# Performance work log

Hardware: AMD Instinct MI355X
Metric: run time of the kernel (lower is better)

Reference implementation:

```python
import jax, jax.numpy as jnp
import numpy as np

N_NODES = 10000
N_EDGES = 80000
N_GRAPHS = 64
H, D = 4, 512          # num_heads, out_feats
EMB = 768
HFEAT = 512
NCLS = 2
SLOPE = 0.2            # DGL GATConv default negative_slope
BN_EPS = 1e-5


def setup_inputs() -> dict:
    key = jax.random.key(0)
    ks = jax.random.split(key, 24)
    f32 = jnp.float32
    rn = lambda k, s, sc=0.02: jax.random.normal(k, s, dtype=f32) * sc
    inp = {
        "node_feat": jax.random.normal(ks[0], (N_NODES, EMB), dtype=f32),
        "func_feat": jax.random.normal(ks[1], (N_NODES, EMB), dtype=f32),
        "W1": rn(ks[2], (EMB, H * D)),
        "al1": rn(ks[3], (H, D), 0.1),
        "ar1": rn(ks[4], (H, D), 0.1),
        "b1": jnp.zeros((H * D,), f32),
        "W2": rn(ks[5], (H * D, H * D)),
        "al2": rn(ks[6], (H, D), 0.1),
        "ar2": rn(ks[7], (H, D), 0.1),
        "b2": jnp.zeros((H * D,), f32),
        "Wfc": rn(ks[8], (H * D, HFEAT)),
        "bfc": jnp.zeros((HFEAT,), f32),
        "Wfco": rn(ks[9], (EMB, HFEAT)),
        "bfco": jnp.zeros((HFEAT,), f32),
        "Wh": rn(ks[10], (8, HFEAT, HFEAT)),
        "bh": jnp.zeros((8, HFEAT), f32),
        "gamma": jnp.ones((HFEAT,), f32),
        "beta": jnp.zeros((HFEAT,), f32),
        "Whfc": rn(ks[11], (HFEAT, HFEAT)),
        "bhfc": jnp.zeros((HFEAT,), f32),
        "Wf": rn(ks[12], (HFEAT, NCLS)),
        "bf": jnp.zeros((NCLS,), f32),
        "src": jax.random.randint(ks[13], (N_EDGES,), 0, N_NODES),
        "dst": jax.random.randint(ks[14], (N_EDGES,), 0, N_NODES),
        "graph_id": jnp.sort(jax.random.randint(ks[15], (N_NODES,), 0, N_GRAPHS)),
    }
    return inp


def gat_conv(h, W, al, ar, b, src, dst):
    """DGL GATConv (eval mode): fc -> per-head attention logits -> edge
    softmax over incoming edges -> scatter-sum -> +bias. Returns (N, H*D)."""
    feat = (h @ W).reshape(-1, H, D)                      # (N,H,D)
    el = jnp.einsum('nhd,hd->nh', feat, al)               # (N,H)
    er = jnp.einsum('nhd,hd->nh', feat, ar)
    e = jax.nn.leaky_relu(el[src] + er[dst], SLOPE)       # (E,H)
    emax = jax.ops.segment_max(e, dst, num_segments=N_NODES)
    ex = jnp.exp(e - emax[dst])
    den = jax.ops.segment_sum(ex, dst, num_segments=N_NODES)
    a = ex / den[dst]                                     # edge softmax (E,H)
    msg = feat[src] * a[:, :, None]                       # (E,H,D) gather+weight
    out = jax.ops.segment_sum(msg, dst, num_segments=N_NODES)
    return (out + b.reshape(1, H, D)).reshape(-1, H * D)


def reference(node_feat, func_feat, W1, al1, ar1, b1, W2, al2, ar2, b2,
              Wfc, bfc, Wfco, bfco, Wh, bh, gamma, beta, Whfc, bhfc,
              Wf, bf, src, dst, graph_id):
    h = gat_conv(node_feat, W1, al1, ar1, b1, src, dst)   # (N, 2048)
    h = gat_conv(h, W2, al2, ar2, b2, src, dst)           # (N, 2048)
    h = jax.nn.elu(h @ Wfc + bfc)                         # (N, 512)
    h_func = jax.nn.elu(func_feat @ Wfco + bfco)          # (N, 512)
    for i in range(8):
        h = jax.nn.elu(h @ Wh[i] + bh[i])
        h_func = jax.nn.elu(h_func @ Wh[i] + bh[i])       # dead for output (as in torch)
    counts = jax.ops.segment_sum(jnp.ones((N_NODES,), h.dtype), graph_id,
                                 num_segments=N_GRAPHS)
    hg = jax.ops.segment_sum(h, graph_id, num_segments=N_GRAPHS)
    hg = hg / jnp.maximum(counts, 1.0)[:, None]           # dgl.mean_nodes (G, 512)
    # BatchNorm1d eval with running_mean=0, running_var=1
    hg = hg / jnp.sqrt(1.0 + BN_EPS) * gamma + beta
    hg = jax.nn.elu(hg @ Whfc + bhfc)
    return hg @ Wf + bf                                   # (G, NCLS)
```

## Files before the change

### kernel.cpp

```cpp
#include <hip/hip_runtime.h>
#include <hip/hip_bf16.h>
#include <math.h>

#define N_NODES 10000
#define N_EDGES 80000
#define N_GRAPHS 64
#define NH 4
#define HD 512
#define HDTOT 2048
#define EMB 768
#define HFEAT 512

typedef _Float16 half8 __attribute__((ext_vector_type(8)));
typedef _Float16 half4 __attribute__((ext_vector_type(4)));
typedef float f32x4 __attribute__((ext_vector_type(4)));

__device__ __forceinline__ void gload_lds16(const void* g, void* l) {
  __builtin_amdgcn_global_load_lds(
      (const __attribute__((address_space(1))) unsigned int*)g,
      (__attribute__((address_space(3))) unsigned int*)l, 16, 0, 0);
}


template <int BM>
__global__ __launch_bounds__(256) void gemm_f16_kernel(
    const _Float16* __restrict__ A, const _Float16* __restrict__ BTs,
    const float* __restrict__ bias, _Float16* __restrict__ C,
    int M, int N, int K, int act) {
  constexpr int WR = (BM == 128) ? 2 : 1;
  constexpr int WC = 4 / WR;
  constexpr int MI = (BM / WR) / 16;
  constexpr int NI = (128 / WC) / 16;

  __shared__ _Float16 As[BM * 32];
  __shared__ _Float16 Bs[128 * 32];

  const int bn = blockIdx.x * 128, bm = blockIdx.y * BM;
  const int t = threadIdx.x;
  const int lane = t & 63, wave = t >> 6;
  const int wr = wave / WC, wc = wave % WC;
  const int m0 = wr * (BM / WR), n0 = wc * (128 / WC);
  const int fr = lane & 15, fq = lane >> 4;

  f32x4 acc[MI][NI];
#pragma unroll
  for (int i = 0; i < MI; ++i)
#pragma unroll
    for (int j = 0; j < NI; ++j) acc[i][j] = (f32x4){0.f, 0.f, 0.f, 0.f};

  for (int k0 = 0; k0 < K; k0 += 32) {
    __syncthreads();
#pragma unroll
    for (int it = 0; it < BM / 64; ++it) {
      int gid = it * 256 + t;
      int r = gid >> 2, q = gid & 3;
      int grow = bm + r;
      if (grow >= M) grow = M - 1;
      half8 v = *(const half8*)(A + (size_t)grow * K + k0 + q * 8);
      *(half8*)&As[r * 32 + (q ^ ((r >> 1) & 3)) * 8] = v;
    }
#pragma unroll
    for (int it = 0; it < 2; ++it) {
      int gid = it * 256 + t;
      int r = gid >> 2, q = gid & 3;
      gload_lds16(BTs + (size_t)(bn + r) * K + k0 + q * 8,
                  &Bs[(it * 256 + wave * 64) * 8]);
    }
    __syncthreads();

    half8 af[MI], bf[NI];
#pragma unroll
    for (int mi = 0; mi < MI; ++mi) {
      int m = m0 + mi * 16 + fr;
      af[mi] = *(const half8*)&As[m * 32 + (fq ^ ((m >> 1) & 3)) * 8];
    }
#pragma unroll
    for (int ni = 0; ni < NI; ++ni) {
      int n = n0 + ni * 16 + fr;
      bf[ni] = *(const half8*)&Bs[n * 32 + (fq ^ ((n >> 1) & 3)) * 8];
    }
#pragma unroll
    for (int mi = 0; mi < MI; ++mi)
#pragma unroll
      for (int ni = 0; ni < NI; ++ni)
        acc[mi][ni] = __builtin_amdgcn_mfma_f32_16x16x32_f16(
            af[mi], bf[ni], acc[mi][ni], 0, 0, 0);
  }
#pragma unroll
  for (int mi = 0; mi < MI; ++mi) {
#pragma unroll
    for (int ni = 0; ni < NI; ++ni) {
      int gcol = bn + n0 + ni * 16 + fr;
      float bb = bias ? bias[gcol] : 0.f;
#pragma unroll
      for (int j = 0; j < 4; ++j) {
        int grow = bm + m0 + mi * 16 + fq * 4 + j;
        if (grow < M) {
          float v = acc[mi][ni][j] + bb;
          if (act == 1) v = v > 0.f ? v : expm1f(v);
          C[(size_t)grow * N + gcol] = (_Float16)v;
        }
      }
    }
  }
}

__global__ __launch_bounds__(256) void hidden_fused_kernel(
    const _Float16* __restrict__ X, const _Float16* __restrict__ Wt,
    const float* __restrict__ bh, _Float16* __restrict__ Y, int M) {
  constexpr int AS = 516;
  __shared__ _Float16 act[32 * AS];
  __shared__ _Float16 Bs[512 * 32];
  const int bm = blockIdx.x * 32;
  const int t = threadIdx.x;
  const int lane = t & 63, wave = t >> 6;
  const int n0w = wave * 128;
  const int fr = lane & 15, fq = lane >> 4;

#pragma unroll
  for (int it = 0; it < 8; ++it) {
    int gid = it * 256 + t;
    int r = gid >> 6, g = gid & 63;
    int grow = bm + r;
    if (grow >= M) grow = M - 1;
    half8 v = *(const half8*)(X + (size_t)grow * HFEAT + g * 8);
    *(half8*)&act[r * AS + g * 8] = v;
  }

  for (int layer = 0; layer < 8; ++layer) {
    const _Float16* W = Wt + (size_t)layer * HFEAT * HFEAT;
    f32x4 acc[2][8];
#pragma unroll
    for (int i = 0; i < 2; ++i)
#pragma unroll
      for (int j = 0; j < 8; ++j) acc[i][j] = (f32x4){0.f, 0.f, 0.f, 0.f};

    for (int k0 = 0; k0 < HFEAT; k0 += 32) {
      __syncthreads();
#pragma unroll
      for (int it = 0; it < 8; ++it) {
        int gid = it * 256 + t;
        int r = gid >> 2, q = gid & 3;
        gload_lds16(W + (size_t)r * HFEAT + k0 + q * 8,
                    &Bs[(it * 256 + wave * 64) * 8]);
      }
      __syncthreads();
      half8 af[2], bf[8];
#pragma unroll
      for (int mi = 0; mi < 2; ++mi)
        af[mi] = *(const half8*)&act[(mi * 16 + fr) * AS + k0 + fq * 8];
#pragma unroll
      for (int ni = 0; ni < 8; ++ni) {
        int n = n0w + ni * 16 + fr;
        bf[ni] = *(const half8*)&Bs[n * 32 + (fq ^ ((n >> 1) & 3)) * 8];
      }
#pragma unroll
      for (int mi = 0; mi < 2; ++mi)
#pragma unroll
        for (int ni = 0; ni < 8; ++ni)
          acc[mi][ni] = __builtin_amdgcn_mfma_f32_16x16x32_f16(
              af[mi], bf[ni], acc[mi][ni], 0, 0, 0);
    }
    __syncthreads();
#pragma unroll
    for (int ni = 0; ni < 8; ++ni) {
      int n = n0w + ni * 16 + fr;
      float bb = bh[layer * HFEAT + n];
#pragma unroll
      for (int mi = 0; mi < 2; ++mi) {
#pragma unroll
        for (int j = 0; j < 4; ++j) {
          int m = mi * 16 + fq * 4 + j;
          float v = acc[mi][ni][j] + bb;
          v = v > 0.f ? v : expm1f(v);
          act[m * AS + n] = (_Float16)v;
        }
      }
    }
  }
  __syncthreads();
#pragma unroll
  for (int it = 0; it < 8; ++it) {
    int gid = it * 256 + t;
    int r = gid >> 6, g = gid & 63;
    if (bm + r < M)
      *(half8*)&Y[(size_t)(bm + r) * HFEAT + g * 8] =
          *(const half8*)&act[r * AS + g * 8];
  }
}

__global__ __launch_bounds__(256) void convert_wt_kernel(
    const float* __restrict__ W, _Float16* __restrict__ WT, int K, int N) {
  __shared__ float tile[32][33];
  W += (size_t)blockIdx.z * K * N;
  WT += (size_t)blockIdx.z * K * N;
  int k0 = blockIdx.x * 32, n0 = blockIdx.y * 32;
  int t = threadIdx.x;
  int r = t >> 3, c4 = (t & 7) * 4;
  float4 v = *(const float4*)(W + (size_t)(k0 + r) * N + n0 + c4);
  tile[r][c4 + 0] = v.x;
  tile[r][c4 + 1] = v.y;
  tile[r][c4 + 2] = v.z;
  tile[r][c4 + 3] = v.w;
  __syncthreads();
  float x0 = tile[c4 + 0][r], x1 = tile[c4 + 1][r];
  float x2 = tile[c4 + 2][r], x3 = tile[c4 + 3][r];
  int n = n0 + r;
  int q = c4 >> 3;
  int s = q ^ ((n >> 1) & 3);
  size_t o = (size_t)n * K + k0 + s * 8 + (c4 & 7);
  *(half4*)&WT[o] = (half4){(_Float16)x0, (_Float16)x1, (_Float16)x2, (_Float16)x3};
}

__global__ void convert_f32_f16_kernel(const float* __restrict__ x,
                                       _Float16* __restrict__ y, int n4) {
  int gid = blockIdx.x * blockDim.x + threadIdx.x;
  if (gid >= n4) return;
  float4 v = *(const float4*)(x + gid * 4);
  *(half4*)(y + gid * 4) =
      (half4){(_Float16)v.x, (_Float16)v.y, (_Float16)v.z, (_Float16)v.w};
}

__global__ void hist_kernel(const int* __restrict__ dst, int* __restrict__ cnt, int E) {
  int gid = blockIdx.x * blockDim.x + threadIdx.x;
  if (gid < E) atomicAdd(&cnt[dst[gid]], 1);
}

__global__ void scan_kernel(const int* __restrict__ cnt, int* __restrict__ row_ptr,
                            int* __restrict__ cursor, int n) {
  __shared__ int part[256];
  int t = threadIdx.x;
  int chunk = (n + 255) / 256;
  int s0 = t * chunk;
  int s1 = min(s0 + chunk, n);
  int sum = 0;
  for (int i = s0; i < s1; ++i) sum += cnt[i];
  part[t] = sum;
  __syncthreads();
  if (t == 0) {
    int acc = 0;
    for (int i = 0; i < 256; ++i) { int v = part[i]; part[i] = acc; acc += v; }
    row_ptr[n] = acc;
  }
  __syncthreads();
  int run = part[t];
  for (int i = s0; i < s1; ++i) {
    row_ptr[i] = run;
    cursor[i] = run;
    run += cnt[i];
  }
}

__global__ void scatter_kernel(const int* __restrict__ dst, int* __restrict__ cursor,
                               int* __restrict__ edge_idx, int E) {
  int gid = blockIdx.x * blockDim.x + threadIdx.x;
  if (gid < E) {
    int pos = atomicAdd(&cursor[dst[gid]], 1);
    edge_idx[pos] = gid;
  }
}

__global__ __launch_bounds__(256) void el_er_kernel(
    const _Float16* __restrict__ feat, const float* __restrict__ al,
    const float* __restrict__ ar, float* __restrict__ el, float* __restrict__ er) {
  int n = blockIdx.x;
  int t = threadIdx.x;
  int h = t >> 6, lane = t & 63;
  half8 f = *(const half8*)(feat + (size_t)n * HDTOT + h * HD + lane * 8);
  const float* ap = al + h * HD + lane * 8;
  const float* rp = ar + h * HD + lane * 8;
  float4 a0 = *(const float4*)ap, a1 = *(const float4*)(ap + 4);
  float4 r0 = *(const float4*)rp, r1 = *(const float4*)(rp + 4);
  float f0 = (float)f[0], f1 = (float)f[1], f2 = (float)f[2], f3 = (float)f[3];
  float f4 = (float)f[4], f5 = (float)f[5], f6 = (float)f[6], f7 = (float)f[7];
  float sl = f0 * a0.x + f1 * a0.y + f2 * a0.z + f3 * a0.w +
             f4 * a1.x + f5 * a1.y + f6 * a1.z + f7 * a1.w;
  float sr = f0 * r0.x + f1 * r0.y + f2 * r0.z + f3 * r0.w +
             f4 * r1.x + f5 * r1.y + f6 * r1.z + f7 * r1.w;
  for (int off = 32; off; off >>= 1) {
    sl += __shfl_down(sl, off);
    sr += __shfl_down(sr, off);
  }
  if (lane == 0) {
    el[n * NH + h] = sl;
    er[n * NH + h] = sr;
  }
}

__global__ void edge_e_kernel(const float* __restrict__ el, const float* __restrict__ er,
                              const int* __restrict__ src, const int* __restrict__ dst,
                              float* __restrict__ e_buf, int EH) {
  int gid = blockIdx.x * blockDim.x + threadIdx.x;
  if (gid >= EH) return;
  int e = gid >> 2, h = gid & 3;
  float v = el[src[e] * NH + h] + er[dst[e] * NH + h];
  e_buf[gid] = v >= 0.f ? v : 0.2f * v;
}

__global__ __launch_bounds__(256) void node_softmax_kernel(
    float* __restrict__ e_buf, const int* __restrict__ row_ptr,
    const int* __restrict__ edge_idx, float* __restrict__ den) {
  int n = blockIdx.x;
  int t = threadIdx.x;
  int h = t >> 6, lane = t & 63;
  int s = row_ptr[n], epos = row_ptr[n + 1];
  if (s == epos) return;
  float m = -INFINITY;
  for (int p = s + lane; p < epos; p += 64) m = fmaxf(m, e_buf[edge_idx[p] * NH + h]);
  for (int off = 32; off; off >>= 1) m = fmaxf(m, __shfl_xor(m, off));
  float sum = 0.f;
  for (int p = s + lane; p < epos; p += 64) {
    int idx = edge_idx[p] * NH + h;
    float ex = expf(e_buf[idx] - m);
    e_buf[idx] = ex;
    sum += ex;
  }
  for (int off = 32; off; off >>= 1) sum += __shfl_xor(sum, off);
  if (lane == 0) den[n * NH + h] = sum;
}

__global__ __launch_bounds__(256) void aggregate_kernel(
    const _Float16* __restrict__ feat, const float* __restrict__ e_buf,
    const float* __restrict__ den, const int* __restrict__ row_ptr,
    const int* __restrict__ edge_idx, const int* __restrict__ src,
    const float* __restrict__ bias, _Float16* __restrict__ out) {
  int n = blockIdx.x;
  int t = threadIdx.x;
  int base = t * 8;
  int h = t >> 6;
  float acc[8] = {0.f, 0.f, 0.f, 0.f, 0.f, 0.f, 0.f, 0.f};
  int s = row_ptr[n], epos = row_ptr[n + 1];
  float inv_den = 0.f;
  if (s < epos) inv_den = 1.f / den[n * NH + h];
  for (int p = s; p < epos; ++p) {
    int e = edge_idx[p];
    int sn = src[e];
    float a = e_buf[e * NH + h] * inv_den;
    half8 f = *(const half8*)(feat + (size_t)sn * HDTOT + base);
#pragma unroll
    for (int i = 0; i < 8; ++i) acc[i] += a * (float)f[i];
  }
  float4 b0 = *(const float4*)(bias + base);
  float4 b1 = *(const float4*)(bias + base + 4);
  half8 o;
  o[0] = (_Float16)(acc[0] + b0.x); o[1] = (_Float16)(acc[1] + b0.y);
  o[2] = (_Float16)(acc[2] + b0.z); o[3] = (_Float16)(acc[3] + b0.w);
  o[4] = (_Float16)(acc[4] + b1.x); o[5] = (_Float16)(acc[5] + b1.y);
  o[6] = (_Float16)(acc[6] + b1.z); o[7] = (_Float16)(acc[7] + b1.w);
  *(half8*)(out + (size_t)n * HDTOT + base) = o;
}

__global__ __launch_bounds__(512) void pool_kernel(
    const _Float16* __restrict__ h, const int* __restrict__ graph_id,
    float* __restrict__ hg, float* __restrict__ counts) {
  int g = blockIdx.x;
  __shared__ int s_lo, s_hi;
  if (threadIdx.x == 0) {
    int lo = 0, hi = N_NODES;
    while (lo < hi) { int m = (lo + hi) >> 1; if (graph_id[m] < g) lo = m + 1; else hi = m; }
    s_lo = lo;
    int lo2 = lo, hi2 = N_NODES;
    while (lo2 < hi2) { int m = (lo2 + hi2) >> 1; if (graph_id[m] < g + 1) lo2 = m + 1; else hi2 = m; }
    s_hi = lo2;
  }
  __syncthreads();
  int lo = s_lo, hi = s_hi;
  int col = threadIdx.x;
  float acc = 0.f;
  for (int n = lo; n < hi; ++n) acc += (float)h[(size_t)n * HFEAT + col];
  hg[g * HFEAT + col] = acc;
  if (col == 0) counts[g] = (float)(hi - lo);
}

__global__ __launch_bounds__(256) void final_kernel(
    const float* __restrict__ hg, const float* __restrict__ counts,
    const float* __restrict__ gamma, const float* __restrict__ beta,
    const float* __restrict__ Whfc, const float* __restrict__ bhfc,
    const float* __restrict__ Wf, const float* __restrict__ bf,
    float* __restrict__ out) {
  __shared__ float sh[HFEAT];
  __shared__ float st[HFEAT];
  __shared__ float r0[4], r1[4];
  int g = blockIdx.x, t = threadIdx.x;
  float invc = 1.f / fmaxf(counts[g], 1.f);
  float bnscale = rsqrtf(1.f + 1e-5f);
  for (int j = t; j < HFEAT; j += 256) {
    float v = hg[g * HFEAT + j] * invc;
    sh[j] = v * bnscale * gamma[j] + beta[j];
  }
  __syncthreads();
  for (int j = t; j < HFEAT; j += 256) {
    float acc = bhfc[j];
    for (int k = 0; k < HFEAT; ++k) acc += sh[k] * Whfc[k * HFEAT + j];
    st[j] = acc > 0.f ? acc : expm1f(acc);
  }
  __syncthreads();
  float p0 = 0.f, p1 = 0.f;
  for (int j = t; j < HFEAT; j += 256) {
    p0 += st[j] * Wf[j * 2 + 0];
    p1 += st[j] * Wf[j * 2 + 1];
  }
  for (int off = 32; off; off >>= 1) {
    p0 += __shfl_down(p0, off);
    p1 += __shfl_down(p1, off);
  }
  int w = t >> 6;
  if ((t & 63) == 0) { r0[w] = p0; r1[w] = p1; }
  __syncthreads();
  if (t == 0) {
    out[g * 2 + 0] = r0[0] + r0[1] + r0[2] + r0[3] + bf[0];
    out[g * 2 + 1] = r1[0] + r1[1] + r1[2] + r1[3] + bf[1];
  }
}

static void gemm(const _Float16* A, const float* W, _Float16* wt,
                 const float* bias, _Float16* C, int M, int N, int K, int act,
                 bool small_m_tile, hipStream_t stream) {
  hipLaunchKernelGGL(convert_wt_kernel, dim3(K / 32, N / 32, 1), dim3(256), 0,
                     stream, W, wt, K, N);
  if (small_m_tile) {
    dim3 grid(N / 128, (M + 63) / 64);
    hipLaunchKernelGGL(gemm_f16_kernel<64>, grid, dim3(256), 0, stream,
                       A, wt, bias, C, M, N, K, act);
  } else {
    dim3 grid(N / 128, (M + 127) / 128);
    hipLaunchKernelGGL(gemm_f16_kernel<128>, grid, dim3(256), 0, stream,
                       A, wt, bias, C, M, N, K, act);
  }
}

static void gat_layer(const _Float16* h_in, int K_in, const float* W, _Float16* wt,
                      const float* al, const float* ar, const float* b,
                      const int* src, const int* dst, const int* row_ptr,
                      const int* edge_idx, _Float16* featbuf, float* el, float* er,
                      float* e_buf, float* den, _Float16* out, hipStream_t stream) {
  gemm(h_in, W, wt, nullptr, featbuf, N_NODES, HDTOT, K_in, 0, false, stream);
  hipLaunchKernelGGL(el_er_kernel, dim3(N_NODES), dim3(256), 0, stream, featbuf, al, ar, el, er);
  int EH = N_EDGES * NH;
  hipLaunchKernelGGL(edge_e_kernel, dim3((EH + 255) / 256), dim3(256), 0, stream,
                     el, er, src, dst, e_buf, EH);
  hipLaunchKernelGGL(node_softmax_kernel, dim3(N_NODES), dim3(256), 0, stream,
                     e_buf, row_ptr, edge_idx, den);
  hipLaunchKernelGGL(aggregate_kernel, dim3(N_NODES), dim3(256), 0, stream,
                     featbuf, e_buf, den, row_ptr, edge_idx, src, b, out);
}

extern "C" void kernel_launch(void* const* d_in, const int* in_sizes, int n_in,
                              void* d_out, int out_size, void* d_ws, size_t ws_size,
                              hipStream_t stream) {
  const float* node_feat = (const float*)d_in[0];
  const float* W1 = (const float*)d_in[2];
  const float* al1 = (const float*)d_in[3];
  const float* ar1 = (const float*)d_in[4];
  const float* b1 = (const float*)d_in[5];
  const float* W2 = (const float*)d_in[6];
  const float* al2 = (const float*)d_in[7];
  const float* ar2 = (const float*)d_in[8];
  const float* b2 = (const float*)d_in[9];
  const float* Wfc = (const float*)d_in[10];
  const float* bfc = (const float*)d_in[11];
  const float* Wh = (const float*)d_in[14];
  const float* bh = (const float*)d_in[15];
  const float* gamma = (const float*)d_in[16];
  const float* beta = (const float*)d_in[17];
  const float* Whfc = (const float*)d_in[18];
  const float* bhfc = (const float*)d_in[19];
  const float* Wf = (const float*)d_in[20];
  const float* bf = (const float*)d_in[21];
  const int* src = (const int*)d_in[22];
  const int* dst = (const int*)d_in[23];
  const int* graph_id = (const int*)d_in[24];
  float* out = (float*)d_out;

  _Float16* P0 = (_Float16*)d_ws;
  _Float16* P1 = P0 + (size_t)N_NODES * HDTOT;
  _Float16* Pin = P1 + (size_t)N_NODES * HDTOT;
  _Float16* wt = Pin + (size_t)N_NODES * EMB;
  _Float16* whh = wt + (size_t)2048 * 2048;
  float* el = (float*)(whh + (size_t)8 * HFEAT * HFEAT);
  float* er = el + N_NODES * NH;
  float* e_buf = er + N_NODES * NH;
  float* den = e_buf + (size_t)N_EDGES * NH;
  float* hg = den + N_NODES * NH;
  float* counts = hg + N_GRAPHS * HFEAT;
  int* cnt = (int*)(counts + N_GRAPHS);
  int* row_ptr = cnt + N_NODES;
  int* cursor = row_ptr + N_NODES + 1;
  int* edge_idx = cursor + N_NODES;

  hipMemsetAsync(cnt, 0, N_NODES * sizeof(int), stream);
  hipLaunchKernelGGL(hist_kernel, dim3((N_EDGES + 255) / 256), dim3(256), 0, stream,
                     dst, cnt, N_EDGES);
  hipLaunchKernelGGL(scan_kernel, dim3(1), dim3(256), 0, stream, cnt, row_ptr, cursor, N_NODES);
  hipLaunchKernelGGL(scatter_kernel, dim3((N_EDGES + 255) / 256), dim3(256), 0, stream,
                     dst, cursor, edge_idx, N_EDGES);

  int n4 = N_NODES * EMB / 4;
  hipLaunchKernelGGL(convert_f32_f16_kernel, dim3((n4 + 255) / 256), dim3(256), 0, stream,
                     node_feat, Pin, n4);
  hipLaunchKernelGGL(convert_wt_kernel, dim3(HFEAT / 32, HFEAT / 32, 8), dim3(256),
                     0, stream, Wh, whh, HFEAT, HFEAT);

  gat_layer(Pin, EMB, W1, wt, al1, ar1, b1, src, dst, row_ptr, edge_idx,
            P0, el, er, e_buf, den, P1, stream);
  gat_layer(P1, HDTOT, W2, wt, al2, ar2, b2, src, dst, row_ptr, edge_idx,
            P0, el, er, e_buf, den, P1, stream);

  gemm(P1, Wfc, wt, bfc, P0, N_NODES, HFEAT, HDTOT, 1, true, stream);

  hipLaunchKernelGGL(hidden_fused_kernel, dim3((N_NODES + 31) / 32), dim3(256),
                     0, stream, P0, whh, bh, P1, N_NODES);

  hipLaunchKernelGGL(pool_kernel, dim3(N_GRAPHS), dim3(512), 0, stream,
                     P1, graph_id, hg, counts);

  hipLaunchKernelGGL(final_kernel, dim3(N_GRAPHS), dim3(256), 0, stream,
                     hg, counts, gamma, beta, Whfc, bhfc, Wf, bf, out);
}
```

Measured before the change: 873.6 us.

## Read hidden-layer weights directly from global memory with 8 waves per block

New measurement: 951.2 us. 1.09x slower.

```diff
diff --git a/kernel.cpp b/kernel.cpp
--- a/kernel.cpp
+++ b/kernel.cpp
@@ -105,65 +105,55 @@
   }
 }
 
-__global__ __launch_bounds__(256) void hidden_fused_kernel(
+__global__ __launch_bounds__(512) void hidden_fused_kernel(
     const _Float16* __restrict__ X, const _Float16* __restrict__ Wt,
     const float* __restrict__ bh, _Float16* __restrict__ Y, int M) {
   constexpr int AS = 516;
   __shared__ _Float16 act[32 * AS];
-  __shared__ _Float16 Bs[512 * 32];
   const int bm = blockIdx.x * 32;
   const int t = threadIdx.x;
   const int lane = t & 63, wave = t >> 6;
-  const int n0w = wave * 128;
+  const int n0w = wave * 64;
   const int fr = lane & 15, fq = lane >> 4;
 
 #pragma unroll
-  for (int it = 0; it < 8; ++it) {
-    int gid = it * 256 + t;
+  for (int it = 0; it < 4; ++it) {
+    int gid = it * 512 + t;
     int r = gid >> 6, g = gid & 63;
     int grow = bm + r;
     if (grow >= M) grow = M - 1;
-    half8 v = *(const half8*)(X + (size_t)grow * HFEAT + g * 8);
-    *(half8*)&act[r * AS + g * 8] = v;
-  }
+    *(half8*)&act[r * AS + g * 8] =
+        *(const half8*)(X + (size_t)grow * HFEAT + g * 8);
+  }
+  __syncthreads();
 
   for (int layer = 0; layer < 8; ++layer) {
     const _Float16* W = Wt + (size_t)layer * HFEAT * HFEAT;
-    f32x4 acc[2][8];
+    f32x4 acc[2][4];
 #pragma unroll
     for (int i = 0; i < 2; ++i)
 #pragma unroll
-      for (int j = 0; j < 8; ++j) acc[i][j] = (f32x4){0.f, 0.f, 0.f, 0.f};
-
+      for (int j = 0; j < 4; ++j) acc[i][j] = (f32x4){0.f, 0.f, 0.f, 0.f};
+
+#pragma unroll
     for (int k0 = 0; k0 < HFEAT; k0 += 32) {
-      __syncthreads();
-#pragma unroll
-      for (int it = 0; it < 8; ++it) {
-        int gid = it * 256 + t;
-        int r = gid >> 2, q = gid & 3;
-        gload_lds16(W + (size_t)r * HFEAT + k0 + q * 8,
-                    &Bs[(it * 256 + wave * 64) * 8]);
-      }
-      __syncthreads();
-      half8 af[2], bf[8];
+      half8 bf[4], af[2];
+#pragma unroll
+      for (int ni = 0; ni < 4; ++ni)
+        bf[ni] = *(const half8*)(W + (size_t)(n0w + ni * 16 + fr) * HFEAT +
+                                 k0 + fq * 8);
+      af[0] = *(const half8*)&act[fr * AS + k0 + fq * 8];
+      af[1] = *(const half8*)&act[(16 + fr) * AS + k0 + fq * 8];
 #pragma unroll
       for (int mi = 0; mi < 2; ++mi)
-        af[mi] = *(const half8*)&act[(mi * 16 + fr) * AS + k0 + fq * 8];
-#pragma unroll
-      for (int ni = 0; ni < 8; ++ni) {
-        int n = n0w + ni * 16 + fr;
-        bf[ni] = *(const half8*)&Bs[n * 32 + (fq ^ ((n >> 1) & 3)) * 8];
-      }
-#pragma unroll
-      for (int mi = 0; mi < 2; ++mi)
-#pragma unroll
-        for (int ni = 0; ni < 8; ++ni)
+#pragma unroll
+        for (int ni = 0; ni < 4; ++ni)
           acc[mi][ni] = __builtin_amdgcn_mfma_f32_16x16x32_f16(
               af[mi], bf[ni], acc[mi][ni], 0, 0, 0);
     }
     __syncthreads();
 #pragma unroll
-    for (int ni = 0; ni < 8; ++ni) {
+    for (int ni = 0; ni < 4; ++ni) {
       int n = n0w + ni * 16 + fr;
       float bb = bh[layer * HFEAT + n];
 #pragma unroll
@@ -177,11 +167,11 @@
         }
       }
     }
-  }
-  __syncthreads();
-#pragma unroll
-  for (int it = 0; it < 8; ++it) {
-    int gid = it * 256 + t;
+    __syncthreads();
+  }
+#pragma unroll
+  for (int it = 0; it < 4; ++it) {
+    int gid = it * 512 + t;
     int r = gid >> 6, g = gid & 63;
     if (bm + r < M)
       *(half8*)&Y[(size_t)(bm + r) * HFEAT + g * 8] =
@@ -189,6 +179,7 @@
   }
 }
 
+template <bool SWZ>
 __global__ __launch_bounds__(256) void convert_wt_kernel(
     const float* __restrict__ W, _Float16* __restrict__ WT, int K, int N) {
   __shared__ float tile[32][33];
@@ -207,7 +198,7 @@
   float x2 = tile[c4 + 2][r], x3 = tile[c4 + 3][r];
   int n = n0 + r;
   int q = c4 >> 3;
-  int s = q ^ ((n >> 1) & 3);
+  int s = SWZ ? (q ^ ((n >> 1) & 3)) : q;
   size_t o = (size_t)n * K + k0 + s * 8 + (c4 & 7);
   *(half4*)&WT[o] = (half4){(_Float16)x0, (_Float16)x1, (_Float16)x2, (_Float16)x3};
 }
@@ -416,8 +407,8 @@
 static void gemm(const _Float16* A, const float* W, _Float16* wt,
                  const float* bias, _Float16* C, int M, int N, int K, int act,
                  bool small_m_tile, hipStream_t stream) {
-  hipLaunchKernelGGL(convert_wt_kernel, dim3(K / 32, N / 32, 1), dim3(256), 0,
-                     stream, W, wt, K, N);
+  hipLaunchKernelGGL(convert_wt_kernel<true>, dim3(K / 32, N / 32, 1), dim3(256),
+                     0, stream, W, wt, K, N);
   if (small_m_tile) {
     dim3 grid(N / 128, (M + 63) / 64);
     hipLaunchKernelGGL(gemm_f16_kernel<64>, grid, dim3(256), 0, stream,
@@ -498,8 +489,8 @@
   int n4 = N_NODES * EMB / 4;
   hipLaunchKernelGGL(convert_f32_f16_kernel, dim3((n4 + 255) / 256), dim3(256), 0, stream,
                      node_feat, Pin, n4);
-  hipLaunchKernelGGL(convert_wt_kernel, dim3(HFEAT / 32, HFEAT / 32, 8), dim3(256),
-                     0, stream, Wh, whh, HFEAT, HFEAT);
+  hipLaunchKernelGGL(convert_wt_kernel<false>, dim3(HFEAT / 32, HFEAT / 32, 8),
+                     dim3(256), 0, stream, Wh, whh, HFEAT, HFEAT);
 
   gat_layer(Pin, EMB, W1, wt, al1, ar1, b1, src, dst, row_ptr, edge_idx,
             P0, el, er, e_buf, den, P1, stream);
@@ -508,7 +499,7 @@
 
   gemm(P1, Wfc, wt, bfc, P0, N_NODES, HFEAT, HDTOT, 1, true, stream);
 
-  hipLaunchKernelGGL(hidden_fused_kernel, dim3((N_NODES + 31) / 32), dim3(256),
+  hipLaunchKernelGGL(hidden_fused_kernel, dim3((N_NODES + 31) / 32), dim3(512),
                      0, stream, P0, whh, bh, P1, N_NODES);
 
   hipLaunchKernelGGL(pool_kernel, dim3(N_GRAPHS), dim3(512), 0, stream,
```
